# Kernel optimization log

Measured on AMD Instinct MI355X. Metric: run time of the kernel, lower is better.

Reference implementation:

```python
import jax, jax.numpy as jnp
import numpy as np

SCALE = 0.5
DROP_P = 0.2

def setup_inputs() -> dict:
    key = jax.random.key(0)
    k1, k2 = jax.random.split(key)
    x1 = jax.random.normal(k1, (8, 2048, 128), dtype=jnp.float32)
    x2 = jax.random.normal(k2, (8, 2048, 128), dtype=jnp.float32)
    return {"x1": x1, "x2": x2}

def reference(x1, x2):
    # scores: [B, M, N] = x1 @ x2^T, scaled by 0.5
    scores = jnp.einsum('bmd,bnd->bmn', x1, x2) * SCALE
    probs = jax.nn.softmax(scores, axis=-1)
    # dropout p=0.2 (training mode in the torch source); fixed key for determinism
    keep = jax.random.bernoulli(jax.random.key(42), 1.0 - DROP_P, probs.shape)
    probs = jnp.where(keep, probs / (1.0 - DROP_P), 0.0)
    # out: [B, M, D] = probs @ x2
    return jnp.einsum('bmn,bnd->bmd', probs, x2)
```

## Files before the change

kernel.cpp:

```cpp
#include <hip/hip_runtime.h>
#include <stdint.h>


typedef __bf16 bf16x8 __attribute__((ext_vector_type(8)));
typedef float f32x4 __attribute__((ext_vector_type(4)));

union FragAB {
  bf16x8 v;
  uint32_t u[4];
};

__device__ __forceinline__ uint32_t rotl32(uint32_t x, uint32_t r) {
  return (x << r) | (x >> (32u - r));
}

__device__ __forceinline__ void threefry2x32_k42(uint32_t in0, uint32_t in1,
                                                 uint32_t& o0, uint32_t& o1) {
  const uint32_t ks0 = 0u;
  const uint32_t ks1 = 42u;
  const uint32_t ks2 = 0x1BD11BDAu ^ 0u ^ 42u;
  uint32_t x0 = in0 + ks0;
  uint32_t x1 = in1 + ks1;
#define TFR(r) { x0 += x1; x1 = rotl32(x1, r); x1 ^= x0; }
  TFR(13u) TFR(15u) TFR(26u) TFR(6u)
  x0 += ks1; x1 += ks2 + 1u;
  TFR(17u) TFR(29u) TFR(16u) TFR(24u)
  x0 += ks2; x1 += ks0 + 2u;
  TFR(13u) TFR(15u) TFR(26u) TFR(6u)
  x0 += ks0; x1 += ks1 + 3u;
  TFR(17u) TFR(29u) TFR(16u) TFR(24u)
  x0 += ks1; x1 += ks2 + 4u;
  TFR(13u) TFR(15u) TFR(26u) TFR(6u)
  x0 += ks2; x1 += ks0 + 5u;
#undef TFR
  o0 = x0; o1 = x1;
}

__device__ __forceinline__ uint32_t pack_bf16(float a, float b) {
  __bf16 ba = (__bf16)a;
  __bf16 bb = (__bf16)b;
  uint32_t ua = (uint32_t)__builtin_bit_cast(uint16_t, ba);
  uint32_t ub = (uint32_t)__builtin_bit_cast(uint16_t, bb);
  return ua | (ub << 16);
}

#define KEEP_LT 3435974144u

__launch_bounds__(256, 2)
__global__ void attn_kernel(const float* __restrict__ x1,
                            const float* __restrict__ x2,
                            float* __restrict__ out) {
  constexpr int LDK = 136;
  constexpr int LDV = 68;
  constexpr int LDP = 72;

  __shared__ __attribute__((aligned(16))) uint16_t Kt[2][64 * LDK];
  __shared__ __attribute__((aligned(16))) uint32_t Vt2[2][64 * LDV];
  __shared__ __attribute__((aligned(16))) uint16_t Pbuf[4][16 * LDP];

  const int tid = threadIdx.x;
  const int wave = tid >> 6;
  const int lane = tid & 63;
  const int l15 = lane & 15;
  const int g = lane >> 4;
  const int half = wave >> 1;
  const int slab = wave & 1;
  const int hid = tid & 127;
  const int b = blockIdx.y;
  const int m0 = blockIdx.x * 32;

  const float QSCALE = 0.5f * 1.44269504088896340736f;
  const int m_arow = m0 + slab * 16 + l15;
  FragAB qf[4];
  const float* qp_base = x1 + ((size_t)b * 2048 + m_arow) * 128;
  #pragma unroll
  for (int c = 0; c < 4; ++c) {
    const float* qp = qp_base + c * 32 + g * 8;
    float4 f0 = *(const float4*)(qp);
    float4 f1 = *(const float4*)(qp + 4);
    qf[c].u[0] = pack_bf16(f0.x * QSCALE, f0.y * QSCALE);
    qf[c].u[1] = pack_bf16(f0.z * QSCALE, f0.w * QSCALE);
    qf[c].u[2] = pack_bf16(f1.x * QSCALE, f1.y * QSCALE);
    qf[c].u[3] = pack_bf16(f1.z * QSCALE, f1.w * QSCALE);
  }

  float m2[4], lsum[4];
  #pragma unroll
  for (int r = 0; r < 4; ++r) { m2[r] = -INFINITY; lsum[r] = 0.0f; }
  f32x4 o[8];
  #pragma unroll
  for (int dt = 0; dt < 8; ++dt) o[dt] = (f32x4){0.f, 0.f, 0.f, 0.f};

  uint32_t rng_row_base[4];
  #pragma unroll
  for (int r = 0; r < 4; ++r)
    rng_row_base[r] = (uint32_t)b * 4194304u +
                      (uint32_t)(m0 + slab * 16 + 4 * g + r) * 2048u + (uint32_t)l15;

  const float* x2b = x2 + (size_t)b * 2048 * 128;
  uint16_t* KtH = &Kt[half][0];
  uint32_t* VtH = &Vt2[half][0];

  for (int ntl = 0; ntl < 16; ++ntl) {
    const int n0 = half * 1024 + ntl * 64;
    __syncthreads();
    #pragma unroll
    for (int i = 0; i < 16; ++i) {
      int f = i * 128 + hid;
      int n = f >> 5;
      int dq = f & 31;
      float4 v = *((const float4*)x2b + (size_t)(n0 + n) * 32 + dq);
      uint32_t p0 = pack_bf16(v.x, v.y);
      uint32_t p1 = pack_bf16(v.z, v.w);
      *(uint2*)&KtH[n * LDK + dq * 4] = make_uint2(p0, p1);
      VtH[(dq * 2 + 0) * LDV + n] = p0;
      VtH[(dq * 2 + 1) * LDV + n] = p1;
    }
    __syncthreads();

    f32x4 s[4];
    #pragma unroll
    for (int t = 0; t < 4; ++t) {
      f32x4 acc = (f32x4){0.f, 0.f, 0.f, 0.f};
      #pragma unroll
      for (int c = 0; c < 4; ++c) {
        FragAB kb;
        uint4 kk = *(const uint4*)&KtH[(t * 16 + l15) * LDK + c * 32 + g * 8];
        kb.u[0] = kk.x; kb.u[1] = kk.y; kb.u[2] = kk.z; kb.u[3] = kk.w;
        acc = __builtin_amdgcn_mfma_f32_16x16x32_bf16(qf[c].v, kb.v, acc, 0, 0, 0);
      }
      s[t] = acc;
    }

    float tmax[4];
    #pragma unroll
    for (int r = 0; r < 4; ++r)
      tmax[r] = fmaxf(fmaxf(s[0][r], s[1][r]), fmaxf(s[2][r], s[3][r]));
    #pragma unroll
    for (int off = 1; off < 16; off <<= 1) {
      #pragma unroll
      for (int r = 0; r < 4; ++r)
        tmax[r] = fmaxf(tmax[r], __shfl_xor(tmax[r], off));
    }
    float alpha[4];
    #pragma unroll
    for (int r = 0; r < 4; ++r) {
      float mn = fmaxf(m2[r], tmax[r]);
      alpha[r] = __builtin_amdgcn_exp2f(m2[r] - mn);
      m2[r] = mn;
    }
    float pvals[4][4];
    float rsum[4] = {0.f, 0.f, 0.f, 0.f};
    #pragma unroll
    for (int t = 0; t < 4; ++t) {
      #pragma unroll
      for (int r = 0; r < 4; ++r) {
        float p = __builtin_amdgcn_exp2f(s[t][r] - m2[r]);
        pvals[t][r] = p;
        rsum[r] += p;
      }
    }
    #pragma unroll
    for (int off = 1; off < 16; off <<= 1) {
      #pragma unroll
      for (int r = 0; r < 4; ++r)
        rsum[r] += __shfl_xor(rsum[r], off);
    }
    #pragma unroll
    for (int r = 0; r < 4; ++r)
      lsum[r] = lsum[r] * alpha[r] + rsum[r];
    #pragma unroll
    for (int dt = 0; dt < 8; ++dt) {
      #pragma unroll
      for (int r = 0; r < 4; ++r)
        o[dt][r] *= alpha[r];
    }

    uint16_t* pb = &Pbuf[wave][0];
    #pragma unroll
    for (int r = 0; r < 4; ++r) {
      uint32_t ibase = rng_row_base[r] + (uint32_t)n0;
      #pragma unroll
      for (int t = 0; t < 4; ++t) {
        uint32_t idx = ibase + t * 16;
        uint32_t o0, o1;
        threefry2x32_k42(0u, idx, o0, o1);
        uint32_t bits = o0 ^ o1;
        float pm = (bits < KEEP_LT) ? pvals[t][r] : 0.0f;
        __bf16 pmb = (__bf16)pm;
        pb[(4 * g + r) * LDP + t * 16 + l15] = __builtin_bit_cast(uint16_t, pmb);
      }
    }

    const uint32_t permsel = (l15 & 1) ? 0x07060302u : 0x05040100u;
    #pragma unroll
    for (int c = 0; c < 2; ++c) {
      FragAB pa;
      uint4 pu = *(const uint4*)&pb[l15 * LDP + c * 32 + g * 8];
      pa.u[0] = pu.x; pa.u[1] = pu.y; pa.u[2] = pu.z; pa.u[3] = pu.w;
      #pragma unroll
      for (int dt = 0; dt < 8; ++dt) {
        int d = dt * 16 + l15;
        const uint32_t* vrow = &VtH[(d >> 1) * LDV + c * 32 + g * 8];
        uint4 U0 = *(const uint4*)vrow;
        uint4 U1 = *(const uint4*)(vrow + 4);
        FragAB vb;
        vb.u[0] = __builtin_amdgcn_perm(U0.y, U0.x, permsel);
        vb.u[1] = __builtin_amdgcn_perm(U0.w, U0.z, permsel);
        vb.u[2] = __builtin_amdgcn_perm(U1.y, U1.x, permsel);
        vb.u[3] = __builtin_amdgcn_perm(U1.w, U1.z, permsel);
        o[dt] = __builtin_amdgcn_mfma_f32_16x16x32_bf16(pa.v, vb.v, o[dt], 0, 0, 0);
      }
    }
  }

  __syncthreads();
  float* comb = (float*)&Kt[0][0];
  if (half == 1) {
    const int src = slab * 64 + lane;
    #pragma unroll
    for (int dt = 0; dt < 8; ++dt)
      #pragma unroll
      for (int r = 0; r < 4; ++r)
        comb[(dt * 4 + r) * 128 + src] = o[dt][r];
    #pragma unroll
    for (int r = 0; r < 4; ++r) {
      comb[(32 + r) * 128 + src] = m2[r];
      comb[(36 + r) * 128 + src] = lsum[r];
    }
  }
  __syncthreads();
  if (half == 0) {
    const int src = slab * 64 + lane;
    float mb[4], lb[4];
    #pragma unroll
    for (int r = 0; r < 4; ++r) {
      mb[r] = comb[(32 + r) * 128 + src];
      lb[r] = comb[(36 + r) * 128 + src];
    }
    float aa[4], ab[4], scale[4];
    #pragma unroll
    for (int r = 0; r < 4; ++r) {
      float ms = fmaxf(m2[r], mb[r]);
      aa[r] = __builtin_amdgcn_exp2f(m2[r] - ms);
      ab[r] = __builtin_amdgcn_exp2f(mb[r] - ms);
      float lt = lsum[r] * aa[r] + lb[r] * ab[r];
      scale[r] = 1.0f / (lt * 0.8f);
    }
    float* ob = out + ((size_t)b * 2048 + m0 + slab * 16 + 4 * g) * 128;
    #pragma unroll
    for (int r = 0; r < 4; ++r) {
      #pragma unroll
      for (int dt = 0; dt < 8; ++dt) {
        float ov = comb[(dt * 4 + r) * 128 + src];
        ob[r * 128 + dt * 16 + l15] = (o[dt][r] * aa[r] + ov * ab[r]) * scale[r];
      }
    }
  }
}

extern "C" void kernel_launch(void* const* d_in, const int* in_sizes, int n_in,
                              void* d_out, int out_size, void* d_ws, size_t ws_size,
                              hipStream_t stream) {
  const float* x1 = (const float*)d_in[0];
  const float* x2 = (const float*)d_in[1];
  float* out = (float*)d_out;
  dim3 grid(64, 8, 1);
  dim3 block(256, 1, 1);
  attn_kernel<<<grid, block, 0, stream>>>(x1, x2, out);
}
```

Measured before the change: 177.2 us.

## Give each wave private K/V tiles to drop block-level barriers

Each wave now loads and converts its own 32-key tile of x2 into private LDS buffers, so the per-iteration __syncthreads pairs become wave-local s_waitcnt. This removes cross-wave barrier stalls. In exchange, each slab pair of waves loads the same K/V data redundantly, which doubles global loads and conversion work. It also halves the tile width and doubles the iteration count.

```diff
diff --git a/kernel.cpp b/kernel.cpp
--- a/kernel.cpp
+++ b/kernel.cpp
@@ -51,23 +51,26 @@
                             const float* __restrict__ x2,
                             float* __restrict__ out) {
   constexpr int LDK = 136;
-  constexpr int LDV = 68;
-  constexpr int LDP = 72;
-
-  __shared__ __attribute__((aligned(16))) uint16_t Kt[2][64 * LDK];
-  __shared__ __attribute__((aligned(16))) uint32_t Vt2[2][64 * LDV];
+  constexpr int LDV = 36;
+  constexpr int LDP = 40;
+
+  __shared__ __attribute__((aligned(16))) uint16_t Kt[4][32 * LDK];
+  __shared__ __attribute__((aligned(16))) uint32_t Vt2[4][64 * LDV];
   __shared__ __attribute__((aligned(16))) uint16_t Pbuf[4][16 * LDP];
 
   const int tid = threadIdx.x;
-  const int wave = tid >> 6;
+  const int wv = __builtin_amdgcn_readfirstlane(tid >> 6);
   const int lane = tid & 63;
   const int l15 = lane & 15;
   const int g = lane >> 4;
-  const int half = wave >> 1;
-  const int slab = wave & 1;
-  const int hid = tid & 127;
+  const int half = wv >> 1;
+  const int slab = wv & 1;
   const int b = blockIdx.y;
   const int m0 = blockIdx.x * 32;
+
+  uint16_t* KtW = &Kt[wv][0];
+  uint32_t* VtW = &Vt2[wv][0];
+  uint16_t* pb = &Pbuf[wv][0];
 
   const float QSCALE = 0.5f * 1.44269504088896340736f;
   const int m_arow = m0 + slab * 16 + l15;
@@ -97,35 +100,33 @@
     rng_row_base[r] = (uint32_t)b * 4194304u +
                       (uint32_t)(m0 + slab * 16 + 4 * g + r) * 2048u + (uint32_t)l15;
 
-  const float* x2b = x2 + (size_t)b * 2048 * 128;
-  uint16_t* KtH = &Kt[half][0];
-  uint32_t* VtH = &Vt2[half][0];
-
-  for (int ntl = 0; ntl < 16; ++ntl) {
-    const int n0 = half * 1024 + ntl * 64;
-    __syncthreads();
+  const float4* x2b4 = (const float4*)(x2 + (size_t)b * 2048 * 128);
+
+  for (int ntl = 0; ntl < 32; ++ntl) {
+    const int n0 = half * 1024 + ntl * 32;
+
     #pragma unroll
     for (int i = 0; i < 16; ++i) {
-      int f = i * 128 + hid;
+      int f = i * 64 + lane;
       int n = f >> 5;
       int dq = f & 31;
-      float4 v = *((const float4*)x2b + (size_t)(n0 + n) * 32 + dq);
+      float4 v = x2b4[(size_t)(n0 + n) * 32 + dq];
       uint32_t p0 = pack_bf16(v.x, v.y);
       uint32_t p1 = pack_bf16(v.z, v.w);
-      *(uint2*)&KtH[n * LDK + dq * 4] = make_uint2(p0, p1);
-      VtH[(dq * 2 + 0) * LDV + n] = p0;
-      VtH[(dq * 2 + 1) * LDV + n] = p1;
-    }
-    __syncthreads();
-
-    f32x4 s[4];
-    #pragma unroll
-    for (int t = 0; t < 4; ++t) {
+      *(uint2*)&KtW[n * LDK + dq * 4] = make_uint2(p0, p1);
+      VtW[dq * LDV + n] = p0;
+      VtW[(dq + 32) * LDV + n] = p1;
+    }
+    asm volatile("s_waitcnt lgkmcnt(0)" ::: "memory");
+
+    f32x4 s[2];
+    #pragma unroll
+    for (int t = 0; t < 2; ++t) {
       f32x4 acc = (f32x4){0.f, 0.f, 0.f, 0.f};
       #pragma unroll
       for (int c = 0; c < 4; ++c) {
         FragAB kb;
-        uint4 kk = *(const uint4*)&KtH[(t * 16 + l15) * LDK + c * 32 + g * 8];
+        uint4 kk = *(const uint4*)&KtW[(t * 16 + l15) * LDK + c * 32 + g * 8];
         kb.u[0] = kk.x; kb.u[1] = kk.y; kb.u[2] = kk.z; kb.u[3] = kk.w;
         acc = __builtin_amdgcn_mfma_f32_16x16x32_bf16(qf[c].v, kb.v, acc, 0, 0, 0);
       }
@@ -135,7 +136,7 @@
     float tmax[4];
     #pragma unroll
     for (int r = 0; r < 4; ++r)
-      tmax[r] = fmaxf(fmaxf(s[0][r], s[1][r]), fmaxf(s[2][r], s[3][r]));
+      tmax[r] = fmaxf(s[0][r], s[1][r]);
     #pragma unroll
     for (int off = 1; off < 16; off <<= 1) {
       #pragma unroll
@@ -149,10 +150,12 @@
       alpha[r] = __builtin_amdgcn_exp2f(m2[r] - mn);
       m2[r] = mn;
     }
-    float pvals[4][4];
-    float rsum[4] = {0.f, 0.f, 0.f, 0.f};
-    #pragma unroll
-    for (int t = 0; t < 4; ++t) {
+    float pvals[2][4];
+    float rsum[4];
+    #pragma unroll
+    for (int r = 0; r < 4; ++r) rsum[r] = 0.f;
+    #pragma unroll
+    for (int t = 0; t < 2; ++t) {
       #pragma unroll
       for (int r = 0; r < 4; ++r) {
         float p = __builtin_amdgcn_exp2f(s[t][r] - m2[r]);
@@ -176,12 +179,11 @@
         o[dt][r] *= alpha[r];
     }
 
-    uint16_t* pb = &Pbuf[wave][0];
     #pragma unroll
     for (int r = 0; r < 4; ++r) {
       uint32_t ibase = rng_row_base[r] + (uint32_t)n0;
       #pragma unroll
-      for (int t = 0; t < 4; ++t) {
+      for (int t = 0; t < 2; ++t) {
         uint32_t idx = ibase + t * 16;
         uint32_t o0, o1;
         threefry2x32_k42(0u, idx, o0, o1);
@@ -191,26 +193,25 @@
         pb[(4 * g + r) * LDP + t * 16 + l15] = __builtin_bit_cast(uint16_t, pmb);
       }
     }
+    asm volatile("s_waitcnt lgkmcnt(0)" ::: "memory");
 
     const uint32_t permsel = (l15 & 1) ? 0x07060302u : 0x05040100u;
-    #pragma unroll
-    for (int c = 0; c < 2; ++c) {
-      FragAB pa;
-      uint4 pu = *(const uint4*)&pb[l15 * LDP + c * 32 + g * 8];
-      pa.u[0] = pu.x; pa.u[1] = pu.y; pa.u[2] = pu.z; pa.u[3] = pu.w;
-      #pragma unroll
-      for (int dt = 0; dt < 8; ++dt) {
-        int d = dt * 16 + l15;
-        const uint32_t* vrow = &VtH[(d >> 1) * LDV + c * 32 + g * 8];
-        uint4 U0 = *(const uint4*)vrow;
-        uint4 U1 = *(const uint4*)(vrow + 4);
-        FragAB vb;
-        vb.u[0] = __builtin_amdgcn_perm(U0.y, U0.x, permsel);
-        vb.u[1] = __builtin_amdgcn_perm(U0.w, U0.z, permsel);
-        vb.u[2] = __builtin_amdgcn_perm(U1.y, U1.x, permsel);
-        vb.u[3] = __builtin_amdgcn_perm(U1.w, U1.z, permsel);
-        o[dt] = __builtin_amdgcn_mfma_f32_16x16x32_bf16(pa.v, vb.v, o[dt], 0, 0, 0);
-      }
+    FragAB pa;
+    uint4 pu = *(const uint4*)&pb[l15 * LDP + g * 8];
+    pa.u[0] = pu.x; pa.u[1] = pu.y; pa.u[2] = pu.z; pa.u[3] = pu.w;
+    #pragma unroll
+    for (int dt = 0; dt < 8; ++dt) {
+      int d = dt * 16 + l15;
+      int rowp = ((d >> 1) & 1) * 32 + (d >> 2);
+      const uint32_t* vrow = &VtW[rowp * LDV + g * 8];
+      uint4 U0 = *(const uint4*)vrow;
+      uint4 U1 = *(const uint4*)(vrow + 4);
+      FragAB vb;
+      vb.u[0] = __builtin_amdgcn_perm(U0.y, U0.x, permsel);
+      vb.u[1] = __builtin_amdgcn_perm(U0.w, U0.z, permsel);
+      vb.u[2] = __builtin_amdgcn_perm(U1.y, U1.x, permsel);
+      vb.u[3] = __builtin_amdgcn_perm(U1.w, U1.z, permsel);
+      o[dt] = __builtin_amdgcn_mfma_f32_16x16x32_bf16(pa.v, vb.v, o[dt], 0, 0, 0);
     }
   }
 
```

New measurement: 214.8 us. +21.2%, slower.
